# Optimization experiments

Hardware: AMD Instinct MI355X
Metric: run time of the kernel (lower is better)

Reference implementation:

```python
import jax, jax.numpy as jnp
import numpy as np

B, S, D = 2, 2048, 2048
HQ, HK, HD = 16, 8, 128          # query heads, kv heads, head_dim
EPS = 1e-6
ROPE_THETA = 10000.0
SCALE = HD ** -0.5


def setup_inputs() -> dict:
    key = jax.random.key(0)
    ks = jax.random.split(key, 6)
    s = lambda fan_in: 1.0 / np.sqrt(fan_in)
    return {
        "hidden_states": jax.random.normal(ks[0], (B, S, D), jnp.float32),
        "positions": jnp.arange(S, dtype=jnp.int32),
        "Wq": jax.random.normal(ks[1], (D, HQ * HD), jnp.float32) * s(D),
        "Wk": jax.random.normal(ks[2], (D, HK * HD), jnp.float32) * s(D),
        "Wv": jax.random.normal(ks[3], (D, HK * HD), jnp.float32) * s(D),
        "Wo": jax.random.normal(ks[4], (HQ * HD, D), jnp.float32) * s(HQ * HD),
        "q_norm_w": jnp.ones((HD,), jnp.float32),
        "k_norm_w": jnp.ones((HD,), jnp.float32),
    }


def _rmsnorm(x, w):
    # RMSNorm over last (head_dim) axis, as in q_norm/k_norm
    var = jnp.mean(jnp.square(x), axis=-1, keepdims=True)
    return x * jax.lax.rsqrt(var + EPS) * w


def _rope(x, positions):
    # x: [B, S, H, HD]; rotate_half-style RoPE (Qwen3 convention)
    half = HD // 2
    inv_freq = 1.0 / (ROPE_THETA ** (jnp.arange(0, half, dtype=jnp.float32) / half))
    angles = positions.astype(jnp.float32)[:, None] * inv_freq[None, :]  # [S, half]
    cos = jnp.cos(angles)[None, :, None, :]  # [1, S, 1, half]
    sin = jnp.sin(angles)[None, :, None, :]
    x1, x2 = x[..., :half], x[..., half:]
    return jnp.concatenate([x1 * cos - x2 * sin, x2 * cos + x1 * sin], axis=-1)


def reference(hidden_states, positions, Wq, Wk, Wv, Wo, q_norm_w, k_norm_w):
    b, s, _ = hidden_states.shape
    q = (hidden_states @ Wq).reshape(b, s, HQ, HD)
    k = (hidden_states @ Wk).reshape(b, s, HK, HD)
    v = (hidden_states @ Wv).reshape(b, s, HK, HD)

    q = _rmsnorm(q, q_norm_w)
    k = _rmsnorm(k, k_norm_w)

    q = _rope(q, positions)
    k = _rope(k, positions)

    # GQA: repeat KV heads to match query heads
    groups = HQ // HK
    k = jnp.repeat(k, groups, axis=2)  # [B, S, HQ, HD]
    v = jnp.repeat(v, groups, axis=2)

    scores = jnp.einsum("bqhd,bkhd->bhqk", q, k) * SCALE  # [B, HQ, S, S]
    causal = jnp.tril(jnp.ones((s, s), dtype=bool))
    scores = jnp.where(causal[None, None], scores, jnp.float32(-jnp.inf))
    attn = jax.nn.softmax(scores, axis=-1)

    out = jnp.einsum("bhqk,bkhd->bqhd", attn, v).reshape(b, s, HQ * HD)
    return out @ Wo
```

## Files before the change

kernel.cpp:

```cpp
#include <hip/hip_runtime.h>
#include <cstdint>
#include <cstddef>

typedef _Float16 half8 __attribute__((ext_vector_type(8)));
typedef _Float16 half4 __attribute__((ext_vector_type(4)));
typedef float f32x4 __attribute__((ext_vector_type(4)));

#define DI __device__ __forceinline__

DI void gld_lds16(void* sp, const void* gp) {
  __builtin_amdgcn_global_load_lds(
      (const __attribute__((address_space(1))) void*)gp,
      (__attribute__((address_space(3))) void*)sp, 16, 0, 0);
}

template <int N>
DI void vmwait() { asm volatile("s_waitcnt vmcnt(%0)" :: "n"(N) : "memory"); }

__global__ __launch_bounds__(256) void prep(const float* __restrict__ hs,
                                            const float* __restrict__ Wq,
                                            const float* __restrict__ Wk,
                                            const float* __restrict__ Wv,
                                            const float* __restrict__ Wo,
                                            _Float16* __restrict__ Xh,
                                            _Float16* __restrict__ Wqkvt,
                                            _Float16* __restrict__ Wot) {
  const int bid = blockIdx.x;
  if (bid >= 12288) {
    const int i = (bid - 12288) * 256 + threadIdx.x;
    const float4* p = (const float4*)hs + (size_t)i * 2;
    const float4 a = p[0], b = p[1];
    half8 h;
    h[0] = (_Float16)a.x; h[1] = (_Float16)a.y; h[2] = (_Float16)a.z; h[3] = (_Float16)a.w;
    h[4] = (_Float16)b.x; h[5] = (_Float16)b.y; h[6] = (_Float16)b.z; h[7] = (_Float16)b.w;
    *(half8*)(Xh + (size_t)i * 8) = h;
    return;
  }
  const float* in;
  _Float16* outp;
  int C, t;
  if (bid < 4096)      { in = Wq; outp = Wqkvt;                        C = 2048; t = bid; }
  else if (bid < 6144) { in = Wk; outp = Wqkvt + (size_t)2048 * 2048;  C = 1024; t = bid - 4096; }
  else if (bid < 8192) { in = Wv; outp = Wqkvt + (size_t)3072 * 2048;  C = 1024; t = bid - 6144; }
  else                 { in = Wo; outp = Wot;                          C = 2048; t = bid - 8192; }
  __shared__ float tl[32][33];
  const int tx = threadIdx.x & 31, ty = threadIdx.x >> 5;
  const int ctiles = C >> 5;
  const int tc = t % ctiles, tr = t / ctiles;
  const int r0 = tr * 32, c0 = tc * 32;
#pragma unroll
  for (int i = 0; i < 4; i++)
    tl[ty + 8 * i][tx] = in[(size_t)(r0 + ty + 8 * i) * C + c0 + tx];
  __syncthreads();
#pragma unroll
  for (int i = 0; i < 4; i++) {
    const int rr = ty + 8 * i;
    outp[(size_t)(c0 + rr) * 2048 + r0 + tx] = (_Float16)tl[tx][rr];
  }
}

template <bool F16OUT>
__global__ __launch_bounds__(256) void gemm_bt(const _Float16* __restrict__ A,
                                               const _Float16* __restrict__ Bt,
                                               void* __restrict__ Cv,
                                               int M, int N, int K) {
  __shared__ _Float16 sA[3][128 * 32];
  __shared__ _Float16 sB[3][128 * 32];
  const int tid = threadIdx.x;
  const int w = tid >> 6, l = tid & 63, lo = l & 15, hi = l >> 4;
  const int gx = gridDim.x, nwg = gx * gridDim.y;
  int bid = blockIdx.y * gx + blockIdx.x;
  bid = (bid & 7) * (nwg >> 3) + (bid >> 3);
  const int bn0 = (bid % gx) * 128, bm0 = (bid / gx) * 128;
  const int wm = w >> 1, wn = w & 1;
  const int srow = l >> 2;
  const int csel = ((l & 3) ^ ((l >> 3) & 3)) * 8;
  const int kswz = (hi ^ ((lo >> 1) & 3)) * 8;

  f32x4 acc[4][4];
#pragma unroll
  for (int mi = 0; mi < 4; mi++)
#pragma unroll
    for (int ni = 0; ni < 4; ni++)
#pragma unroll
      for (int r = 0; r < 4; r++) acc[mi][ni][r] = 0.0f;

  auto stage = [&](int kt, int bi) {
#pragma unroll
    for (int i = 0; i < 2; ++i) {
      const int j = 2 * w + i;
      gld_lds16(&sA[bi][j * 512],
                A + (size_t)(bm0 + j * 16 + srow) * K + (size_t)kt * 32 + csel);
      gld_lds16(&sB[bi][j * 512],
                Bt + (size_t)(bn0 + j * 16 + srow) * K + (size_t)kt * 32 + csel);
    }
  };

  stage(0, 0);
  stage(1, 1);
  vmwait<4>();
  __builtin_amdgcn_s_barrier();
  const int KT = K >> 5;
  int cur = 0;
#pragma unroll 1
  for (int kt = 0; kt < KT; ++kt) {
    const int nxt = (cur == 0) ? 2 : cur - 1;
    if (kt + 2 < KT) stage(kt + 2, nxt);
    half8 a[4], b[4];
#pragma unroll
    for (int mi = 0; mi < 4; mi++)
      a[mi] = *(const half8*)&sA[cur][(wm * 64 + mi * 16 + lo) * 32 + kswz];
#pragma unroll
    for (int ni = 0; ni < 4; ni++)
      b[ni] = *(const half8*)&sB[cur][(wn * 64 + ni * 16 + lo) * 32 + kswz];
#pragma unroll
    for (int mi = 0; mi < 4; mi++)
#pragma unroll
      for (int ni = 0; ni < 4; ni++)
        acc[mi][ni] = __builtin_amdgcn_mfma_f32_16x16x32_f16(a[mi], b[ni], acc[mi][ni], 0, 0, 0);
    if (kt + 2 < KT) vmwait<4>();
    else if (kt + 2 == KT) vmwait<0>();
    __builtin_amdgcn_s_barrier();
    cur = (cur == 2) ? 0 : cur + 1;
  }

#pragma unroll
  for (int mi = 0; mi < 4; mi++)
#pragma unroll
    for (int ni = 0; ni < 4; ni++)
#pragma unroll
      for (int r = 0; r < 4; r++) {
        const size_t idx = (size_t)(bm0 + wm * 64 + mi * 16 + hi * 4 + r) * N +
                           (bn0 + wn * 64 + ni * 16 + lo);
        if constexpr (F16OUT) ((_Float16*)Cv)[idx] = (_Float16)acc[mi][ni][r];
        else                  ((float*)Cv)[idx] = acc[mi][ni][r];
      }
}

__global__ __launch_bounds__(256) void post(const _Float16* __restrict__ QKV,
                                            const int* __restrict__ pos,
                                            const float* __restrict__ qw,
                                            const float* __restrict__ kw,
                                            _Float16* __restrict__ Qb,
                                            _Float16* __restrict__ Kb,
                                            _Float16* __restrict__ Vt) {
  if (blockIdx.x >= 24576) {
    __shared__ _Float16 tt[32][33];
    const int g = blockIdx.x - 24576;
    const int tx = threadIdx.x & 31, ty = threadIdx.x >> 5;
    const int dt = g & 3;
    const int st = (g >> 2) & 63;
    const int bh = g >> 8;
    const _Float16* src = QKV + (size_t)((bh >> 3) * 2048 + st * 32) * 4096 +
                          3072 + (bh & 7) * 128 + dt * 32;
#pragma unroll
    for (int i = 0; i < 4; i++)
      tt[ty + 8 * i][tx] = src[(size_t)(ty + 8 * i) * 4096 + tx];
    __syncthreads();
    _Float16* dst = Vt + ((size_t)bh * 128 + dt * 32) * 2048 + st * 32;
#pragma unroll
    for (int i = 0; i < 4; i++) {
      const int rr = ty + 8 * i;
      dst[(size_t)rr * 2048 + tx] = tt[tx][rr];
    }
    return;
  }
  const int w = threadIdx.x >> 6, l = threadIdx.x & 63;
  const int wv = blockIdx.x * 4 + w;
  const int t = wv / 24, hh = wv - t * 24;
  const int b = t >> 11, s = t & 2047;
  const bool isq = hh < 16;
  const int col = isq ? hh * 128 : 2048 + (hh - 16) * 128;
  const _Float16* x = QKV + (size_t)t * 4096 + col;
  const float x1 = (float)x[l], x2 = (float)x[l + 64];
  float ss = x1 * x1 + x2 * x2;
  ss += __shfl_xor(ss, 32); ss += __shfl_xor(ss, 16); ss += __shfl_xor(ss, 8);
  ss += __shfl_xor(ss, 4);  ss += __shfl_xor(ss, 2);  ss += __shfl_xor(ss, 1);
  const float rn = rsqrtf(ss * 0.0078125f + 1e-6f);
  const float* wt = isq ? qw : kw;
  const float n1 = x1 * rn * wt[l], n2 = x2 * rn * wt[l + 64];
  const float ang = (float)pos[s] * exp2f((float)l * -0.2076205059304601f);
  float sa, ca;
  sincosf(ang, &sa, &ca);
  const float qs = isq ? 0.12751731f : 1.0f;
  const float o1 = (n1 * ca - n2 * sa) * qs;
  const float o2 = (n2 * ca + n1 * sa) * qs;
  _Float16* dst = isq ? Qb + (((size_t)b * 16 + hh) * 2048 + s) * 128
                      : Kb + (((size_t)b * 8 + (hh - 16)) * 2048 + s) * 128;
  dst[l] = (_Float16)o1;
  dst[l + 64] = (_Float16)o2;
}

__global__ __launch_bounds__(256) void attn_fwd(const _Float16* __restrict__ Q,
                                                const _Float16* __restrict__ K,
                                                const _Float16* __restrict__ Vt,
                                                _Float16* __restrict__ AO) {
  __shared__ _Float16 sK[2][64 * 128];
  __shared__ _Float16 sV[2][128 * 64];
  __shared__ _Float16 P[4][16 * 80];
  const int tid = threadIdx.x, w = tid >> 6, l = tid & 63, lo = l & 15, hi = l >> 4;
  const int qt = 31 - (blockIdx.x >> 5);
  const int hq = blockIdx.x & 15;
  const int b = (blockIdx.x >> 4) & 1;
  const int hk = hq >> 1, q0 = qt * 64;
  const _Float16* Qh = Q + ((size_t)(b * 16 + hq) * 2048) * 128;
  const _Float16* Kh = K + ((size_t)(b * 8 + hk) * 2048) * 128;
  const _Float16* Vh = Vt + ((size_t)(b * 8 + hk) * 128) * 2048;
  const int qw0 = q0 + w * 16;

  auto stageK = [&](int bi, int kv0) {
#pragma unroll
    for (int i = 0; i < 4; ++i) {
      const int inst = w * 4 + i;
      const int r = inst * 4 + (l >> 4);
      const int cb = ((l & 15) * 16) ^ ((r & 7) << 4);
      gld_lds16(&sK[bi][inst * 512],
                (const char*)Kh + (size_t)(kv0 + r) * 256 + cb);
    }
  };
  auto stageV = [&](int bi, int kv0) {
#pragma unroll
    for (int i = 0; i < 4; ++i) {
      const int inst = w * 4 + i;
      const int r = inst * 8 + (l >> 3);
      const int cb = ((l & 7) * 16) ^ ((r & 7) << 4);
      gld_lds16(&sV[bi][inst * 512],
                (const char*)Vh + (size_t)r * 4096 + (size_t)kv0 * 2 + cb);
    }
  };

  half8 aq[4];
#pragma unroll
  for (int kc = 0; kc < 4; kc++)
    aq[kc] = *(const half8*)(Qh + (size_t)(qw0 + lo) * 128 + kc * 32 + hi * 8);

  f32x4 o[8];
#pragma unroll
  for (int dn = 0; dn < 8; dn++)
#pragma unroll
    for (int r = 0; r < 4; r++) o[dn][r] = 0.0f;
  float mrow = -1e30f, lrow = 0.0f;

  const int nt = qt + 1;
  stageK(0, 0);
  stageV(0, 0);
  __syncthreads();
#pragma unroll 1
  for (int kt = 0; kt < nt; ++kt) {
    const int kv0 = kt * 64;
    const int cur = kt & 1;
    if (kt + 1 < nt) {
      stageK(cur ^ 1, kv0 + 64);
      stageV(cur ^ 1, kv0 + 64);
    }
    const char* kb = (const char*)sK[cur];
    const char* vb = (const char*)sV[cur];
    f32x4 s[4];
#pragma unroll
    for (int ns = 0; ns < 4; ns++) {
#pragma unroll
      for (int r = 0; r < 4; r++) s[ns][r] = 0.0f;
      const int krow = ns * 16 + lo;
#pragma unroll
      for (int kc = 0; kc < 4; kc++) {
        half8 bk = *(const half8*)(kb + krow * 256 +
                                   ((kc * 64 + hi * 16) ^ ((krow & 7) << 4)));
        s[ns] = __builtin_amdgcn_mfma_f32_16x16x32_f16(bk, aq[kc], s[ns], 0, 0, 0);
      }
    }
    if (kt == nt - 1) {
#pragma unroll
      for (int ns = 0; ns < 4; ns++) {
        const int kv = kv0 + ns * 16 + hi * 4;
#pragma unroll
        for (int r = 0; r < 4; r++)
          if (kv + r > qw0 + lo) s[ns][r] = -1e30f;
      }
    }
    float tmax = s[0][0];
#pragma unroll
    for (int ns = 0; ns < 4; ns++)
#pragma unroll
      for (int r = 0; r < 4; r++) tmax = fmaxf(tmax, s[ns][r]);
    tmax = fmaxf(tmax, __shfl_xor(tmax, 16));
    tmax = fmaxf(tmax, __shfl_xor(tmax, 32));
    if (!__all(tmax <= mrow + 8.0f)) {
      const float mn = fmaxf(mrow, tmax);
      const float corr = exp2f(mrow - mn);
      mrow = mn;
      lrow *= corr;
      float c4[4];
#pragma unroll
      for (int r = 0; r < 4; r++) c4[r] = __shfl(corr, hi * 4 + r, 16);
#pragma unroll
      for (int dn = 0; dn < 8; dn++)
#pragma unroll
        for (int r = 0; r < 4; r++) o[dn][r] *= c4[r];
    }
    float psum = 0.0f;
#pragma unroll
    for (int ns = 0; ns < 4; ns++) {
      half4 pk;
#pragma unroll
      for (int r = 0; r < 4; r++) {
        const float p = exp2f(s[ns][r] - mrow);
        psum += p;
        pk[r] = (_Float16)p;
      }
      *(half4*)&P[w][lo * 80 + ns * 16 + hi * 4] = pk;
    }
    psum += __shfl_xor(psum, 16);
    psum += __shfl_xor(psum, 32);
    lrow += psum;
    asm volatile("s_waitcnt lgkmcnt(0)" ::: "memory");
    half8 ap0 = *(const half8*)&P[w][lo * 80 + hi * 8];
    half8 ap1 = *(const half8*)&P[w][lo * 80 + 32 + hi * 8];
#pragma unroll
    for (int dn = 0; dn < 8; dn++) {
      const int vrow = dn * 16 + lo;
      half8 bv0 = *(const half8*)(vb + vrow * 128 + ((hi * 16) ^ ((vrow & 7) << 4)));
      half8 bv1 = *(const half8*)(vb + vrow * 128 + ((64 + hi * 16) ^ ((vrow & 7) << 4)));
      o[dn] = __builtin_amdgcn_mfma_f32_16x16x32_f16(ap0, bv0, o[dn], 0, 0, 0);
      o[dn] = __builtin_amdgcn_mfma_f32_16x16x32_f16(ap1, bv1, o[dn], 0, 0, 0);
    }
    __syncthreads();
  }

  const float inv = 1.0f / lrow;
  float i4[4];
#pragma unroll
  for (int r = 0; r < 4; r++) i4[r] = __shfl(inv, hi * 4 + r, 16);
  const size_t tok = (size_t)b * 2048 + qw0;
#pragma unroll
  for (int dn = 0; dn < 8; dn++)
#pragma unroll
    for (int r = 0; r < 4; r++)
      AO[(tok + hi * 4 + r) * 2048 + hq * 128 + dn * 16 + lo] = (_Float16)(o[dn][r] * i4[r]);
}

extern "C" void kernel_launch(void* const* d_in, const int* in_sizes, int n_in,
                              void* d_out, int out_size, void* d_ws, size_t ws_size,
                              hipStream_t stream) {
  (void)in_sizes; (void)n_in; (void)out_size; (void)ws_size;
  const float* hs  = (const float*)d_in[0];
  const int*   pos = (const int*)d_in[1];
  const float* Wq  = (const float*)d_in[2];
  const float* Wk  = (const float*)d_in[3];
  const float* Wv  = (const float*)d_in[4];
  const float* Wo  = (const float*)d_in[5];
  const float* qnw = (const float*)d_in[6];
  const float* knw = (const float*)d_in[7];
  float* out = (float*)d_out;

  char* ws = (char*)d_ws;
  size_t off = 0;
  auto take = [&](size_t bytes) -> void* {
    void* p = ws + off;
    off += (bytes + 255) & ~(size_t)255;
    return p;
  };
  _Float16* Xh    = (_Float16*)take((size_t)4096 * 2048 * 2);
  _Float16* Wqkvt = (_Float16*)take((size_t)4096 * 2048 * 2);
  _Float16* Wot   = (_Float16*)take((size_t)2048 * 2048 * 2);
  _Float16* QKVh  = (_Float16*)take((size_t)4096 * 4096 * 2);
  _Float16* Qb    = (_Float16*)take((size_t)2 * 16 * 2048 * 128 * 2);
  _Float16* Kb    = (_Float16*)take((size_t)2 * 8 * 2048 * 128 * 2);
  _Float16* Vt    = (_Float16*)take((size_t)2 * 8 * 128 * 2048 * 2);
  _Float16* AO    = (_Float16*)take((size_t)4096 * 2048 * 2);

  prep<<<16384, 256, 0, stream>>>(hs, Wq, Wk, Wv, Wo, Xh, Wqkvt, Wot);
  gemm_bt<true><<<dim3(32, 32), 256, 0, stream>>>(Xh, Wqkvt, QKVh, 4096, 4096, 2048);
  post<<<28672, 256, 0, stream>>>(QKVh, pos, qnw, knw, Qb, Kb, Vt);
  attn_fwd<<<1024, 256, 0, stream>>>(Qb, Kb, Vt, AO);
  gemm_bt<false><<<dim3(16, 32), 256, 0, stream>>>(AO, Wot, out, 4096, 2048, 2048);
}
```

Before: 263.6 us.

## Template GEMM on M tile, use 64-row tiles for output projection, double-buffer

```diff
diff --git a/kernel.cpp b/kernel.cpp
--- a/kernel.cpp
+++ b/kernel.cpp
@@ -13,9 +13,6 @@
       (const __attribute__((address_space(1))) void*)gp,
       (__attribute__((address_space(3))) void*)sp, 16, 0, 0);
 }
-
-template <int N>
-DI void vmwait() { asm volatile("s_waitcnt vmcnt(%0)" :: "n"(N) : "memory"); }
 
 __global__ __launch_bounds__(256) void prep(const float* __restrict__ hs,
                                             const float* __restrict__ Wq,
@@ -59,78 +56,78 @@
   }
 }
 
-template <bool F16OUT>
+template <int BM, bool F16OUT>
 __global__ __launch_bounds__(256) void gemm_bt(const _Float16* __restrict__ A,
                                                const _Float16* __restrict__ Bt,
                                                void* __restrict__ Cv,
                                                int M, int N, int K) {
-  __shared__ _Float16 sA[3][128 * 32];
-  __shared__ _Float16 sB[3][128 * 32];
+  constexpr int MF = BM / 32;
+  constexpr int LA = BM / 64;
+  __shared__ _Float16 sA[2][BM * 32];
+  __shared__ _Float16 sB[2][128 * 32];
   const int tid = threadIdx.x;
   const int w = tid >> 6, l = tid & 63, lo = l & 15, hi = l >> 4;
   const int gx = gridDim.x, nwg = gx * gridDim.y;
   int bid = blockIdx.y * gx + blockIdx.x;
   bid = (bid & 7) * (nwg >> 3) + (bid >> 3);
-  const int bn0 = (bid % gx) * 128, bm0 = (bid / gx) * 128;
+  const int bn0 = (bid % gx) * 128, bm0 = (bid / gx) * BM;
   const int wm = w >> 1, wn = w & 1;
   const int srow = l >> 2;
   const int csel = ((l & 3) ^ ((l >> 3) & 3)) * 8;
   const int kswz = (hi ^ ((lo >> 1) & 3)) * 8;
 
-  f32x4 acc[4][4];
-#pragma unroll
-  for (int mi = 0; mi < 4; mi++)
+  f32x4 acc[MF][4];
+#pragma unroll
+  for (int mi = 0; mi < MF; mi++)
 #pragma unroll
     for (int ni = 0; ni < 4; ni++)
 #pragma unroll
       for (int r = 0; r < 4; r++) acc[mi][ni][r] = 0.0f;
 
-  auto stage = [&](int kt, int bi) {
+  auto stage = [&](int bi, int kt) {
+#pragma unroll
+    for (int i = 0; i < LA; ++i) {
+      const int j = LA * w + i;
+      gld_lds16(&sA[bi][j * 512],
+                A + (size_t)(bm0 + j * 16 + srow) * K + (size_t)kt * 32 + csel);
+    }
 #pragma unroll
     for (int i = 0; i < 2; ++i) {
       const int j = 2 * w + i;
-      gld_lds16(&sA[bi][j * 512],
-                A + (size_t)(bm0 + j * 16 + srow) * K + (size_t)kt * 32 + csel);
       gld_lds16(&sB[bi][j * 512],
                 Bt + (size_t)(bn0 + j * 16 + srow) * K + (size_t)kt * 32 + csel);
     }
   };
 
   stage(0, 0);
-  stage(1, 1);
-  vmwait<4>();
-  __builtin_amdgcn_s_barrier();
+  __syncthreads();
   const int KT = K >> 5;
-  int cur = 0;
 #pragma unroll 1
   for (int kt = 0; kt < KT; ++kt) {
-    const int nxt = (cur == 0) ? 2 : cur - 1;
-    if (kt + 2 < KT) stage(kt + 2, nxt);
-    half8 a[4], b[4];
-#pragma unroll
-    for (int mi = 0; mi < 4; mi++)
-      a[mi] = *(const half8*)&sA[cur][(wm * 64 + mi * 16 + lo) * 32 + kswz];
+    const int cur = kt & 1;
+    if (kt + 1 < KT) stage(cur ^ 1, kt + 1);
+    half8 a[MF], b[4];
+#pragma unroll
+    for (int mi = 0; mi < MF; mi++)
+      a[mi] = *(const half8*)&sA[cur][(wm * (BM / 2) + mi * 16 + lo) * 32 + kswz];
 #pragma unroll
     for (int ni = 0; ni < 4; ni++)
       b[ni] = *(const half8*)&sB[cur][(wn * 64 + ni * 16 + lo) * 32 + kswz];
 #pragma unroll
-    for (int mi = 0; mi < 4; mi++)
+    for (int mi = 0; mi < MF; mi++)
 #pragma unroll
       for (int ni = 0; ni < 4; ni++)
         acc[mi][ni] = __builtin_amdgcn_mfma_f32_16x16x32_f16(a[mi], b[ni], acc[mi][ni], 0, 0, 0);
-    if (kt + 2 < KT) vmwait<4>();
-    else if (kt + 2 == KT) vmwait<0>();
-    __builtin_amdgcn_s_barrier();
-    cur = (cur == 2) ? 0 : cur + 1;
-  }
-
-#pragma unroll
-  for (int mi = 0; mi < 4; mi++)
+    __syncthreads();
+  }
+
+#pragma unroll
+  for (int mi = 0; mi < MF; mi++)
 #pragma unroll
     for (int ni = 0; ni < 4; ni++)
 #pragma unroll
       for (int r = 0; r < 4; r++) {
-        const size_t idx = (size_t)(bm0 + wm * 64 + mi * 16 + hi * 4 + r) * N +
+        const size_t idx = (size_t)(bm0 + wm * (BM / 2) + mi * 16 + hi * 4 + r) * N +
                            (bn0 + wn * 64 + ni * 16 + lo);
         if constexpr (F16OUT) ((_Float16*)Cv)[idx] = (_Float16)acc[mi][ni][r];
         else                  ((float*)Cv)[idx] = acc[mi][ni][r];
@@ -369,8 +366,8 @@
   _Float16* AO    = (_Float16*)take((size_t)4096 * 2048 * 2);
 
   prep<<<16384, 256, 0, stream>>>(hs, Wq, Wk, Wv, Wo, Xh, Wqkvt, Wot);
-  gemm_bt<true><<<dim3(32, 32), 256, 0, stream>>>(Xh, Wqkvt, QKVh, 4096, 4096, 2048);
+  gemm_bt<128, true><<<dim3(32, 32), 256, 0, stream>>>(Xh, Wqkvt, QKVh, 4096, 4096, 2048);
   post<<<28672, 256, 0, stream>>>(QKVh, pos, qnw, knw, Qb, Kb, Vt);
   attn_fwd<<<1024, 256, 0, stream>>>(Qb, Kb, Vt, AO);
-  gemm_bt<false><<<dim3(16, 32), 256, 0, stream>>>(AO, Wot, out, 4096, 2048, 2048);
-}
+  gemm_bt<64, false><<<dim3(16, 64), 256, 0, stream>>>(AO, Wot, out, 4096, 2048, 2048);
+}
```

Result: no change. 261.3 us (-0.9%).
